# Kernel tuning notes

Hardware: AMD Instinct MI355X
Metric: run time of the kernel (lower is better)

## Reference

```python
import jax, jax.numpy as jnp
import numpy as np

H = 12          # attention heads
NUM_LAYERS = 2  # encoder depth
SCALE = 0.02    # weight init scale


def _ln(x, g, b):
    m = jnp.mean(x, axis=-1, keepdims=True)
    v = jnp.mean((x - m) ** 2, axis=-1, keepdims=True)
    return (x - m) * jax.lax.rsqrt(v + 1e-5) * g + b


def _split_heads(t):
    b, n, d = t.shape
    return t.reshape(b, n, H, d // H).transpose(0, 2, 1, 3)  # (b, h, n, dh)


def _block(p, x, h):
    """Encoder1DBlock: pre-LN elu-linear attention + MLP; returns (x_out, new_hidden)."""
    (lnig, lnib, lnhg, lnhb, lnog, lnob,
     Wqkv, bqkv, Wqkvh, bqkvh, Wout, bout, W1, b1, W2, b2) = p
    xn = _ln(x, lnig, lnib)
    hn = _ln(h, lnhg, lnhb)
    qkv = xn @ Wqkv + bqkv + hn @ Wqkvh + bqkvh            # (b, n, 3d)
    q, k, v = jnp.split(qkv, 3, axis=-1)
    q = jax.nn.elu(_split_heads(q)) + 1.0
    k = jax.nn.elu(_split_heads(k)) + 1.0
    v = _split_heads(v)
    # linear attention: (q k^T) v == q (k^T v); skip the n x n matrix
    kv = jnp.einsum('bhjd,bhje->bhde', k, v)
    o = jnp.einsum('bhid,bhde->bhie', q, kv)
    o = o.transpose(0, 2, 1, 3).reshape(x.shape)
    attn = o @ Wout + bout                                  # to_out
    x2 = attn + x
    y = jax.nn.gelu(_ln(x2, lnog, lnob) @ W1 + b1, approximate=False) @ W2 + b2
    return x2 + y, attn + h


def _encoder(x, hidden, spatial_pos, temporal_pos, params):
    # pos[b,t,j,d] = temporal[b,t,d] * spatial[b,j,d]  (the n=1 einsum in the source)
    pos = temporal_pos[:, :, None, :] * spatial_pos[:, None, :, :]  # (b, L, n, d)
    for idx in range(NUM_LAYERS):
        x = x + pos
        x_t = jnp.moveaxis(x, 1, 0)          # (L, b, n, d)
        # forward direction: hidden gets pos_embedding[:, idx] (layer index, as in source)
        pf = tuple(p[0, idx] for p in params)
        pos_f = pos[:, idx]
        def step_f(h, xt, pf=pf, pos_f=pos_f):
            y, h2 = _block(pf, xt, h + pos_f)
            return h2, y
        _, yf = jax.lax.scan(step_f, hidden, x_t)
        # backward direction: hidden gets the time-indexed pos of the current frame
        pb = tuple(p[1, idx] for p in params)
        pos_t = jnp.moveaxis(pos, 1, 0)
        def step_b(h, inp, pb=pb):
            xt, pt = inp
            y, h2 = _block(pb, xt, h + pt)
            return h2, y
        _, yb = jax.lax.scan(step_b, hidden, (x_t[::-1], pos_t[::-1]))
        x = jnp.moveaxis(yf + yb[::-1], 0, 1)
    return x


def setup_inputs() -> dict:
    key = jax.random.key(0)
    B, L, N, D, M = 2, 12, 1024, 768, 3072
    ks = jax.random.split(key, 16)
    P = (2, NUM_LAYERS)  # (direction, layer)
    w = lambda k, shape: jax.random.normal(k, shape, jnp.float32) * SCALE
    inp = {
        'x': jax.random.normal(ks[0], (B, L, N, D), jnp.float32),
        'hidden': jax.random.normal(ks[1], (B, N, D), jnp.float32),
        'spatial_pos': jax.random.normal(ks[2], (B, N, D), jnp.float32) * 0.02,
        'temporal_pos': jax.random.normal(ks[3], (B, L, D), jnp.float32),
        'lni_g': jnp.ones(P + (D,)), 'lni_b': jnp.zeros(P + (D,)),
        'lnh_g': jnp.ones(P + (D,)), 'lnh_b': jnp.zeros(P + (D,)),
        'lno_g': jnp.ones(P + (D,)), 'lno_b': jnp.zeros(P + (D,)),
        'Wqkv': w(ks[4], P + (D, 3 * D)), 'bqkv': jnp.zeros(P + (3 * D,)),
        'Wqkvh': w(ks[5], P + (D, 3 * D)), 'bqkvh': jnp.zeros(P + (3 * D,)),
        'Wout': w(ks[6], P + (D, D)), 'bout': jnp.zeros(P + (D,)),
        'W1': w(ks[7], P + (D, M)), 'b1': jnp.zeros(P + (M,)),
        'W2': w(ks[8], P + (M, D)), 'b2': jnp.zeros(P + (D,)),
    }
    return inp


def reference(x, hidden, spatial_pos, temporal_pos,
              lni_g, lni_b, lnh_g, lnh_b, lno_g, lno_b,
              Wqkv, bqkv, Wqkvh, bqkvh, Wout, bout, W1, b1, W2, b2):
    params = (lni_g, lni_b, lnh_g, lnh_b, lno_g, lno_b,
              Wqkv, bqkv, Wqkvh, bqkvh, Wout, bout, W1, b1, W2, b2)
    return _encoder(x, hidden, spatial_pos, temporal_pos, params)
```

## Files before the change

kernel.cpp:

```cpp
#include <hip/hip_runtime.h>

#define DEV __device__ __forceinline__
typedef unsigned short u16;
typedef __attribute__((ext_vector_type(8))) __bf16 bf16x8;
typedef __attribute__((ext_vector_type(4))) float f32x4;

constexpr int Ln = 12, Nn = 1024, Dn = 768;

DEV float bf2f(u16 u) { unsigned x = ((unsigned)u) << 16; return __builtin_bit_cast(float, x); }
DEV u16 f2bf(float f) {
    unsigned x = __builtin_bit_cast(unsigned, f);
    x = (x + 0x7fffu + ((x >> 16) & 1u)) >> 16;
    return (u16)x;
}

DEV void gll16(const u16* g, u16* l) {
    __builtin_amdgcn_global_load_lds((const __attribute__((address_space(1))) unsigned*)g,
                                     (__attribute__((address_space(3))) unsigned*)l, 16, 0, 0);
}

DEV float block_sum(float v, float* sred) {
#pragma unroll
    for (int o = 32; o > 0; o >>= 1) v += __shfl_down(v, o, 64);
    int wid = threadIdx.x >> 6, lane = threadIdx.x & 63;
    if (lane == 0) sred[wid] = v;
    __syncthreads();
    v = sred[0] + sred[1] + sred[2] + sred[3];
    __syncthreads();
    return v;
}

__global__ void __launch_bounds__(256) ln1_kernel(
    const float* __restrict__ xf, const u16* __restrict__ xb, float* __restrict__ hbuf,
    const float* __restrict__ temporal, const float* __restrict__ spatial,
    const float* __restrict__ lig, const float* __restrict__ lib,
    const float* __restrict__ lhg, const float* __restrict__ lhb,
    u16* __restrict__ acat, int l, int tF, int tB)
{
    __shared__ float sred[4];
    int r = blockIdx.x, tid = threadIdx.x;
    int dir = r >> 11, b = (r >> 10) & 1, n = r & 1023;
    int t = dir ? tB : tF;
    int tp = dir ? tB : l;
    int so = (dir * 2 + l) * Dn;
    size_t xoff = ((size_t)(b * Ln + t) * Nn + n) * Dn;
    float* hrow = hbuf + (size_t)r * Dn;
    const float* trt = temporal + (size_t)(b * Ln + t) * Dn;
    const float* trh = temporal + (size_t)(b * Ln + tp) * Dn;
    const float* srow = spatial + (size_t)(b * Nn + n) * Dn;
    u16* arow = acat + (size_t)r * (2 * Dn);

    float xv[3], hv[3], sx = 0.f, sh = 0.f;
#pragma unroll
    for (int i = 0; i < 3; i++) {
        int c = tid + i * 256;
        float sp = srow[c];
        float xr = xf ? xf[xoff + c] : bf2f(xb[xoff + c]);
        xv[i] = xr + trt[c] * sp;
        hv[i] = hrow[c] + trh[c] * sp;
        hrow[c] = hv[i];
        sx += xv[i]; sh += hv[i];
    }
    float mx = block_sum(sx, sred) * (1.f / 768.f);
    float mh = block_sum(sh, sred) * (1.f / 768.f);
    float vx = 0.f, vh = 0.f;
#pragma unroll
    for (int i = 0; i < 3; i++) {
        float d = xv[i] - mx; vx += d * d;
        d = hv[i] - mh; vh += d * d;
    }
    vx = block_sum(vx, sred) * (1.f / 768.f);
    vh = block_sum(vh, sred) * (1.f / 768.f);
    float rx = rsqrtf(vx + 1e-5f), rh = rsqrtf(vh + 1e-5f);
#pragma unroll
    for (int i = 0; i < 3; i++) {
        int c = tid + i * 256;
        arow[c]      = f2bf((xv[i] - mx) * rx * lig[so + c] + lib[so + c]);
        arow[Dn + c] = f2bf((hv[i] - mh) * rh * lhg[so + c] + lhb[so + c]);
    }
}

__global__ void __launch_bounds__(256) ln2_kernel(
    const float* __restrict__ x2, const float* __restrict__ g, const float* __restrict__ bb,
    u16* __restrict__ out, int l)
{
    __shared__ float sred[4];
    int r = blockIdx.x, tid = threadIdx.x;
    int dir = r >> 11;
    int so = (dir * 2 + l) * Dn;
    const float* row = x2 + (size_t)r * Dn;
    u16* orow = out + (size_t)r * Dn;
    float v[3], s = 0.f;
#pragma unroll
    for (int i = 0; i < 3; i++) { int c = tid + i * 256; v[i] = row[c]; s += v[i]; }
    float m = block_sum(s, sred) * (1.f / 768.f);
    float va = 0.f;
#pragma unroll
    for (int i = 0; i < 3; i++) { float d = v[i] - m; va += d * d; }
    va = block_sum(va, sred) * (1.f / 768.f);
    float rs = rsqrtf(va + 1e-5f);
#pragma unroll
    for (int i = 0; i < 3; i++) {
        int c = tid + i * 256;
        orow[c] = f2bf((v[i] - m) * rs * g[so + c] + bb[so + c]);
    }
}

struct GArgs {
    const u16* A; int lda;
    const u16* BT; long long bstride; int ldb; int K;
    const float* Wf; const float* Wf2; long long wstride; int ksplit;
    const float* bias1; int b1s;
    const float* bias2; int b2s;
    u16* obf;
    const float* xf; const u16* xb;
    u16* yb; float* yf; int store_flag;
    const float* temp; const float* spat;
    float* x2; float* hbuf;
    int tF, tB;
};

template <int MT, int NT, int MODE, bool CACHED>
__global__ void __launch_bounds__(256) gemm_kernel(GArgs ga)
{
    __shared__ __align__(16) u16 As[MT * 32];
    __shared__ __align__(16) u16 Bs[NT * 32];
    constexpr int FM = MT / 32, FN = NT / 32;
    int tid = threadIdx.x;
    const u16 *A, *Bc = nullptr;
    const float *W1_ = nullptr, *W2_ = nullptr;
    int lda, ldb, K, rowbase, colbase, dir = 0;
    if constexpr (MODE == 1) {
        int combo = blockIdx.y, g4 = combo / 12, h = combo - g4 * 12;
        rowbase = g4 * 1024 + blockIdx.x * MT; colbase = h * 64;
        A = ga.A + (size_t)rowbase * 2304 + h * 64; lda = 2304;
        Bc = ga.BT + (size_t)combo * 4096; ldb = 64; K = 64;
    } else {
        dir = blockIdx.z;
        rowbase = dir * 2048 + blockIdx.x * MT; colbase = blockIdx.y * NT;
        A = ga.A + (size_t)rowbase * ga.lda; lda = ga.lda;
        ldb = ga.ldb; K = ga.K;
        if constexpr (CACHED) {
            Bc = ga.BT + (size_t)dir * ga.bstride + (size_t)colbase * ldb;
        } else {
            W1_ = ga.Wf + (size_t)dir * ga.wstride + colbase;
            if (ga.Wf2) W2_ = ga.Wf2 + (size_t)dir * ga.wstride + colbase;
        }
    }
    int wid = tid >> 6, lane = tid & 63;
    int wm = wid >> 1, wn = wid & 1, lrow = lane & 15, kq = lane >> 4;
    f32x4 acc[FM][FN];
#pragma unroll
    for (int i = 0; i < FM; i++)
#pragma unroll
        for (int j = 0; j < FN; j++) acc[i][j] = f32x4{0.f, 0.f, 0.f, 0.f};

    for (int k0 = 0; k0 < K; k0 += 32) {
#pragma unroll
        for (int p = 0; p < (MT * 64) / 4096; p++) {
            int idx = p * 256 + tid, row = idx >> 2, ch = idx & 3;
            gll16(A + (size_t)row * lda + k0 + ch * 8, As + idx * 8);
        }
        if constexpr (CACHED || MODE == 1) {
#pragma unroll
            for (int p = 0; p < (NT * 64) / 4096; p++) {
                int idx = p * 256 + tid, row = idx >> 2, ch = idx & 3;
                gll16(Bc + (size_t)row * ldb + k0 + ch * 8, Bs + idx * 8);
            }
        } else {
            const float* Wk = (W2_ && k0 >= ga.ksplit) ? W2_ + (size_t)(k0 - ga.ksplit) * ldb
                                                       : W1_ + (size_t)k0 * ldb;
#pragma unroll
            for (int p = 0; p < NT / 32; p++) {
                int u = p * 256 + tid;
                int k = u >> 5, nb = u & 31;
                float4 w = *(const float4*)(Wk + (size_t)k * ldb + nb * 4);
                Bs[(nb * 4 + 0) * 32 + k] = f2bf(w.x);
                Bs[(nb * 4 + 1) * 32 + k] = f2bf(w.y);
                Bs[(nb * 4 + 2) * 32 + k] = f2bf(w.z);
                Bs[(nb * 4 + 3) * 32 + k] = f2bf(w.w);
            }
        }
        __syncthreads();
        bf16x8 av[FM], bv[FN];
#pragma unroll
        for (int i = 0; i < FM; i++)
            av[i] = *(const bf16x8*)(As + (wm * (MT / 2) + i * 16 + lrow) * 32 + kq * 8);
#pragma unroll
        for (int j = 0; j < FN; j++)
            bv[j] = *(const bf16x8*)(Bs + (wn * (NT / 2) + j * 16 + lrow) * 32 + kq * 8);
#pragma unroll
        for (int i = 0; i < FM; i++)
#pragma unroll
            for (int j = 0; j < FN; j++)
                acc[i][j] = __builtin_amdgcn_mfma_f32_16x16x32_bf16(av[i], bv[j], acc[i][j], 0, 0, 0);
        __syncthreads();
    }

    const float* b1 = ga.bias1 ? ga.bias1 + (size_t)dir * ga.b1s : nullptr;
    const float* b2 = ga.bias2 ? ga.bias2 + (size_t)dir * ga.b2s : nullptr;
#pragma unroll
    for (int fm = 0; fm < FM; fm++) {
#pragma unroll
        for (int fn = 0; fn < FN; fn++) {
#pragma unroll
            for (int r2 = 0; r2 < 4; r2++) {
                int row = rowbase + wm * (MT / 2) + fm * 16 + kq * 4 + r2;
                int col = colbase + wn * (NT / 2) + fn * 16 + lrow;
                float v = acc[fm][fn][r2];
                if constexpr (MODE == 0) {
                    v += b1[col] + b2[col];
                    if (col < 1536) v = v > 0.f ? v + 1.f : __expf(v);
                    ga.obf[(size_t)row * 2304 + col] = f2bf(v);
                } else if constexpr (MODE == 1) {
                    ga.obf[(size_t)row * 768 + col] = f2bf(v);
                } else if constexpr (MODE == 2) {
                    v += b1[col];
                    int b = (row >> 10) & 1, n = row & 1023;
                    int t = (row >> 11) ? ga.tB : ga.tF;
                    float pos = ga.temp[(size_t)(b * Ln + t) * Dn + col] *
                                ga.spat[(size_t)(b * Nn + n) * Dn + col];
                    size_t xi = ((size_t)(b * Ln + t) * Nn + n) * Dn + col;
                    float xv = (ga.xf ? ga.xf[xi] : bf2f(ga.xb[xi])) + pos;
                    ga.x2[(size_t)row * Dn + col] = v + xv;
                    ga.hbuf[(size_t)row * Dn + col] += v;
                } else if constexpr (MODE == 3) {
                    v += b1[col];
                    v = 0.5f * v * (1.f + erff(v * 0.7071067811865475f));
                    ga.obf[(size_t)row * 3072 + col] = f2bf(v);
                } else {
                    v += b1[col] + ga.x2[(size_t)row * Dn + col];
                    int b = (row >> 10) & 1, n = row & 1023;
                    int t = (row >> 11) ? ga.tB : ga.tF;
                    size_t oi = ((size_t)(b * Ln + t) * Nn + n) * Dn + col;
                    if (ga.yf) {
                        if (ga.store_flag) ga.yf[oi] = v;
                        else ga.yf[oi] += v;
                    } else {
                        if (ga.store_flag) ga.yb[oi] = f2bf(v);
                        else ga.yb[oi] = f2bf(v + bf2f(ga.yb[oi]));
                    }
                }
            }
        }
    }
}

__global__ void __launch_bounds__(256) kv_partial_kernel(const u16* __restrict__ qkv,
                                                         float* __restrict__ part)
{
    int combo = blockIdx.x, js = blockIdx.y;
    int g4 = combo / 12, h = combo - g4 * 12;
    int d0 = (threadIdx.x & 15) * 4, e0 = (threadIdx.x >> 4) * 4;
    const u16* base = qkv + ((size_t)g4 * 1024 + js * 128) * 2304 + 768 + h * 64;
    float acc[4][4] = {};
#pragma unroll 4
    for (int j = 0; j < 128; j++) {
        const u16* kp = base + (size_t)j * 2304 + d0;
        const u16* vp = base + (size_t)j * 2304 + 768 + e0;
        ushort4 kk = *(const ushort4*)kp;
        ushort4 vv = *(const ushort4*)vp;
        float kd[4] = {bf2f(kk.x), bf2f(kk.y), bf2f(kk.z), bf2f(kk.w)};
        float ve[4] = {bf2f(vv.x), bf2f(vv.y), bf2f(vv.z), bf2f(vv.w)};
#pragma unroll
        for (int di = 0; di < 4; di++)
#pragma unroll
            for (int ei = 0; ei < 4; ei++) acc[di][ei] += kd[di] * ve[ei];
    }
    float* pp = part + ((size_t)js * 48 + combo) * 4096;
#pragma unroll
    for (int di = 0; di < 4; di++)
#pragma unroll
        for (int ei = 0; ei < 4; ei++)
            pp[(e0 + ei) * 64 + (d0 + di)] = acc[di][ei];
}

__global__ void __launch_bounds__(256) kv_reduce_kernel(const float* __restrict__ part,
                                                        u16* __restrict__ kvT)
{
    int combo = blockIdx.x;
    for (int idx = threadIdx.x; idx < 4096; idx += 256) {
        float s = 0.f;
#pragma unroll
        for (int js = 0; js < 8; js++) s += part[((size_t)js * 48 + combo) * 4096 + idx];
        kvT[(size_t)combo * 4096 + idx] = f2bf(s);
    }
}

__global__ void transpose_kernel(const float* __restrict__ src, u16* __restrict__ dst,
                                 int K, int N, int ldd, int dcol)
{
    __shared__ float tile[32][33];
    int n0 = blockIdx.x * 32, k0 = blockIdx.y * 32;
    int tx = threadIdx.x, ty = threadIdx.y;
#pragma unroll
    for (int i = 0; i < 4; i++) {
        int k = k0 + ty + i * 8;
        tile[ty + i * 8][tx] = src[(size_t)k * N + n0 + tx];
    }
    __syncthreads();
#pragma unroll
    for (int i = 0; i < 4; i++) {
        int n = n0 + ty + i * 8;
        dst[(size_t)n * ldd + dcol + k0 + tx] = f2bf(tile[tx][ty + i * 8]);
    }
}

__global__ void __launch_bounds__(256) init_h_kernel(const float* __restrict__ hidden,
                                                     float* __restrict__ hbuf)
{
    unsigned i = blockIdx.x * 256u + threadIdx.x;
    unsigned d = i % 768u;
    unsigned r = i / 768u;
    unsigned b = (r >> 10) & 1u, n = r & 1023u;
    hbuf[i] = hidden[((size_t)b * 1024 + n) * 768 + d];
}

extern "C" void kernel_launch(void* const* d_in, const int* in_sizes, int n_in,
                              void* d_out, int out_size, void* d_ws, size_t ws_size,
                              hipStream_t stream)
{
    (void)in_sizes; (void)n_in; (void)out_size;
    const float* xin    = (const float*)d_in[0];
    const float* hidden = (const float*)d_in[1];
    const float* spat   = (const float*)d_in[2];
    const float* temp   = (const float*)d_in[3];
    const float* lig    = (const float*)d_in[4];
    const float* lib_   = (const float*)d_in[5];
    const float* lhg    = (const float*)d_in[6];
    const float* lhb    = (const float*)d_in[7];
    const float* log_   = (const float*)d_in[8];
    const float* lob    = (const float*)d_in[9];
    const float* Wqkv   = (const float*)d_in[10];
    const float* bqkv   = (const float*)d_in[11];
    const float* Wqkvh  = (const float*)d_in[12];
    const float* bqkvh  = (const float*)d_in[13];
    const float* Wout   = (const float*)d_in[14];
    const float* bout   = (const float*)d_in[15];
    const float* W1     = (const float*)d_in[16];
    const float* b1     = (const float*)d_in[17];
    const float* W2     = (const float*)d_in[18];
    const float* b2     = (const float*)d_in[19];

    char* w = (char*)d_ws;
    float* hbuf  = (float*)(w + 0);
    float* x2    = (float*)(w + 12582912);
    u16*   xC    = (u16*)(w + 25165824);
    u16*   kvT   = (u16*)(w + 62914560);
    u16*   regA  = (u16*)(w + 63307776);
    u16*   regB  = (u16*)(w + 75890688);
    u16*   qkvTc = (u16*)(w + 101056512);
    u16*   woutTc= (u16*)(w + 115212288);
    u16*   w1Tc  = (u16*)(w + 117571584);
    u16*   w2Tc  = (u16*)(w + 127008768);
    const bool cached = ws_size >= 136445952ull;

    u16*   acat  = regA;
    float* kvp   = (float*)regA;
    u16*   obf   = regA;
    u16*   ln2b  = regA + 3145728;
    u16*   qkvb  = regB;
    u16*   mlp1b = regB;

    dim3 tb(32, 8);
    for (int l = 0; l < 2; l++) {
        if (cached) {
            for (int dir = 0; dir < 2; dir++) {
                int s4 = dir * 2 + l;
                transpose_kernel<<<dim3(72, 24), tb, 0, stream>>>(
                    Wqkv + (size_t)s4 * 768 * 2304, qkvTc + (size_t)dir * 2304 * 1536, 768, 2304, 1536, 0);
                transpose_kernel<<<dim3(72, 24), tb, 0, stream>>>(
                    Wqkvh + (size_t)s4 * 768 * 2304, qkvTc + (size_t)dir * 2304 * 1536, 768, 2304, 1536, 768);
                transpose_kernel<<<dim3(24, 24), tb, 0, stream>>>(
                    Wout + (size_t)s4 * 768 * 768, woutTc + (size_t)dir * 768 * 768, 768, 768, 768, 0);
                transpose_kernel<<<dim3(96, 24), tb, 0, stream>>>(
                    W1 + (size_t)s4 * 768 * 3072, w1Tc + (size_t)dir * 3072 * 768, 768, 3072, 768, 0);
                transpose_kernel<<<dim3(24, 96), tb, 0, stream>>>(
                    W2 + (size_t)s4 * 3072 * 768, w2Tc + (size_t)dir * 768 * 3072, 3072, 768, 3072, 0);
            }
        }
        init_h_kernel<<<12288, 256, 0, stream>>>(hidden, hbuf);
        const float* xsf = l ? nullptr : xin;
        const u16*   xsb = l ? xC : nullptr;
        float* yf = l ? (float*)d_out : nullptr;
        u16*   yb = l ? nullptr : xC;
        for (int s = 0; s < 12; s++) {
            int tF = s, tB = 11 - s;
            ln1_kernel<<<4096, 256, 0, stream>>>(xsf, xsb, hbuf, temp, spat, lig, lib_, lhg, lhb,
                                                 acat, l, tF, tB);
            {
                GArgs g{};
                g.A = acat; g.lda = 1536; g.K = 1536;
                g.bias1 = bqkv + (size_t)l * 2304; g.b1s = 2 * 2304;
                g.bias2 = bqkvh + (size_t)l * 2304; g.b2s = 2 * 2304;
                g.obf = qkvb;
                if (cached) {
                    g.BT = qkvTc; g.bstride = 2304ll * 1536; g.ldb = 1536;
                    gemm_kernel<128, 128, 0, true><<<dim3(16, 18, 2), 256, 0, stream>>>(g);
                } else {
                    g.Wf = Wqkv + (size_t)l * 768 * 2304;
                    g.Wf2 = Wqkvh + (size_t)l * 768 * 2304;
                    g.wstride = 2ll * 768 * 2304; g.ksplit = 768; g.ldb = 2304;
                    gemm_kernel<128, 128, 0, false><<<dim3(16, 18, 2), 256, 0, stream>>>(g);
                }
            }
            kv_partial_kernel<<<dim3(48, 8), 256, 0, stream>>>(qkvb, kvp);
            kv_reduce_kernel<<<48, 256, 0, stream>>>(kvp, kvT);
            {
                GArgs g{};
                g.A = qkvb; g.BT = kvT; g.obf = obf;
                gemm_kernel<128, 64, 1, true><<<dim3(8, 48, 1), 256, 0, stream>>>(g);
            }
            {
                GArgs g{};
                g.A = obf; g.lda = 768; g.K = 768;
                g.bias1 = bout + (size_t)l * 768; g.b1s = 2 * 768;
                g.xf = xsf; g.xb = xsb; g.temp = temp; g.spat = spat; g.x2 = x2; g.hbuf = hbuf;
                g.tF = tF; g.tB = tB;
                if (cached) {
                    g.BT = woutTc; g.bstride = 768ll * 768; g.ldb = 768;
                    gemm_kernel<128, 128, 2, true><<<dim3(16, 6, 2), 256, 0, stream>>>(g);
                } else {
                    g.Wf = Wout + (size_t)l * 768 * 768; g.wstride = 2ll * 768 * 768;
                    g.ldb = 768; g.ksplit = g.K;
                    gemm_kernel<128, 128, 2, false><<<dim3(16, 6, 2), 256, 0, stream>>>(g);
                }
            }
            ln2_kernel<<<4096, 256, 0, stream>>>(x2, log_, lob, ln2b, l);
            {
                GArgs g{};
                g.A = ln2b; g.lda = 768; g.K = 768;
                g.bias1 = b1 + (size_t)l * 3072; g.b1s = 2 * 3072;
                g.obf = mlp1b;
                if (cached) {
                    g.BT = w1Tc; g.bstride = 3072ll * 768; g.ldb = 768;
                    gemm_kernel<128, 128, 3, true><<<dim3(16, 24, 2), 256, 0, stream>>>(g);
                } else {
                    g.Wf = W1 + (size_t)l * 768 * 3072; g.wstride = 2ll * 768 * 3072;
                    g.ldb = 3072; g.ksplit = g.K;
                    gemm_kernel<128, 128, 3, false><<<dim3(16, 24, 2), 256, 0, stream>>>(g);
                }
            }
            {
                GArgs g{};
                g.A = mlp1b; g.lda = 3072; g.K = 3072;
                g.bias1 = b2 + (size_t)l * 768; g.b1s = 2 * 768;
                g.x2 = x2; g.yf = yf; g.yb = yb; g.store_flag = (s <= 5) ? 1 : 0;
                g.tF = tF; g.tB = tB;
                if (cached) {
                    g.BT = w2Tc; g.bstride = 768ll * 3072; g.ldb = 3072;
                    gemm_kernel<128, 128, 4, true><<<dim3(16, 6, 2), 256, 0, stream>>>(g);
                } else {
                    g.Wf = W2 + (size_t)l * 3072 * 768; g.wstride = 2ll * 3072 * 768;
                    g.ldb = 768; g.ksplit = g.K;
                    gemm_kernel<128, 128, 4, false><<<dim3(16, 6, 2), 256, 0, stream>>>(g);
                }
            }
        }
    }
}
```

Before: 6.983 ms.

## Double-buffer LDS tiles in cached GEMM path to overlap loads with MFMA

For GEMM variants whose B operand is already bf16 (cached weights or the per-head kv mode), the kernel now keeps two LDS buffers. It issues direct global-to-LDS loads for the next K-step before computing on the current one, and uses an explicit vmcnt wait plus barriers. This is meant to hide global memory latency behind the MFMA work. The cost is twice the LDS footprint for those variants, which may lower occupancy. The uncached fp32-weight path stays single-buffered.

```diff
diff --git a/kernel.cpp b/kernel.cpp
--- a/kernel.cpp
+++ b/kernel.cpp
@@ -123,9 +123,11 @@
 template <int MT, int NT, int MODE, bool CACHED>
 __global__ void __launch_bounds__(256) gemm_kernel(GArgs ga)
 {
-    __shared__ __align__(16) u16 As[MT * 32];
-    __shared__ __align__(16) u16 Bs[NT * 32];
     constexpr int FM = MT / 32, FN = NT / 32;
+    constexpr bool DB = (CACHED || MODE == 1);
+    constexpr int NBUF = DB ? 2 : 1;
+    __shared__ __align__(16) u16 As[NBUF][MT * 32];
+    __shared__ __align__(16) u16 Bs[NBUF][NT * 32];
     int tid = threadIdx.x;
     const u16 *A, *Bc = nullptr;
     const float *W1_ = nullptr, *W2_ = nullptr;
@@ -155,46 +157,85 @@
 #pragma unroll
         for (int j = 0; j < FN; j++) acc[i][j] = f32x4{0.f, 0.f, 0.f, 0.f};
 
-    for (int k0 = 0; k0 < K; k0 += 32) {
-#pragma unroll
-        for (int p = 0; p < (MT * 64) / 4096; p++) {
-            int idx = p * 256 + tid, row = idx >> 2, ch = idx & 3;
-            gll16(A + (size_t)row * lda + k0 + ch * 8, As + idx * 8);
+    if constexpr (DB) {
+        constexpr int AL = (MT * 64) / 4096;
+        constexpr int BL = (NT * 64) / 4096;
+        constexpr int LPS = AL + BL;
+        auto stage = [&](int buf, int k0) {
+#pragma unroll
+            for (int p = 0; p < AL; p++) {
+                int idx = p * 256 + tid, row = idx >> 2, ch = idx & 3;
+                gll16(A + (size_t)row * lda + k0 + ch * 8, As[buf] + idx * 8);
+            }
+#pragma unroll
+            for (int p = 0; p < BL; p++) {
+                int idx = p * 256 + tid, row = idx >> 2, ch = idx & 3;
+                gll16(Bc + (size_t)row * ldb + k0 + ch * 8, Bs[buf] + idx * 8);
+            }
+        };
+        stage(0, 0);
+        const int nk = K >> 5;
+        for (int t = 0; t < nk; t++) {
+            int cur = t & 1;
+            if (t + 1 < nk) {
+                stage(cur ^ 1, (t + 1) << 5);
+                asm volatile("s_waitcnt vmcnt(%0)" :: "n"(LPS) : "memory");
+            } else {
+                asm volatile("s_waitcnt vmcnt(0)" ::: "memory");
+            }
+            __builtin_amdgcn_s_barrier();
+            asm volatile("" ::: "memory");
+            bf16x8 av[FM], bv[FN];
+#pragma unroll
+            for (int i = 0; i < FM; i++)
+                av[i] = *(const bf16x8*)(As[cur] + (wm * (MT / 2) + i * 16 + lrow) * 32 + kq * 8);
+#pragma unroll
+            for (int j = 0; j < FN; j++)
+                bv[j] = *(const bf16x8*)(Bs[cur] + (wn * (NT / 2) + j * 16 + lrow) * 32 + kq * 8);
+#pragma unroll
+            for (int i = 0; i < FM; i++)
+#pragma unroll
+                for (int j = 0; j < FN; j++)
+                    acc[i][j] = __builtin_amdgcn_mfma_f32_16x16x32_bf16(av[i], bv[j], acc[i][j], 0, 0, 0);
+            asm volatile("" ::: "memory");
+            __builtin_amdgcn_s_barrier();
         }
-        if constexpr (CACHED || MODE == 1) {
-#pragma unroll
-            for (int p = 0; p < (NT * 64) / 4096; p++) {
+    } else {
+        for (int k0 = 0; k0 < K; k0 += 32) {
+#pragma unroll
+            for (int p = 0; p < (MT * 64) / 4096; p++) {
                 int idx = p * 256 + tid, row = idx >> 2, ch = idx & 3;
-                gll16(Bc + (size_t)row * ldb + k0 + ch * 8, Bs + idx * 8);
-            }
-        } else {
-            const float* Wk = (W2_ && k0 >= ga.ksplit) ? W2_ + (size_t)(k0 - ga.ksplit) * ldb
-                                                       : W1_ + (size_t)k0 * ldb;
-#pragma unroll
-            for (int p = 0; p < NT / 32; p++) {
-                int u = p * 256 + tid;
-                int k = u >> 5, nb = u & 31;
-                float4 w = *(const float4*)(Wk + (size_t)k * ldb + nb * 4);
-                Bs[(nb * 4 + 0) * 32 + k] = f2bf(w.x);
-                Bs[(nb * 4 + 1) * 32 + k] = f2bf(w.y);
-                Bs[(nb * 4 + 2) * 32 + k] = f2bf(w.z);
-                Bs[(nb * 4 + 3) * 32 + k] = f2bf(w.w);
-            }
+                gll16(A + (size_t)row * lda + k0 + ch * 8, As[0] + idx * 8);
+            }
+            {
+                const float* Wk = (W2_ && k0 >= ga.ksplit) ? W2_ + (size_t)(k0 - ga.ksplit) * ldb
+                                                           : W1_ + (size_t)k0 * ldb;
+#pragma unroll
+                for (int p = 0; p < NT / 32; p++) {
+                    int u = p * 256 + tid;
+                    int k = u >> 5, nb = u & 31;
+                    float4 w = *(const float4*)(Wk + (size_t)k * ldb + nb * 4);
+                    Bs[0][(nb * 4 + 0) * 32 + k] = f2bf(w.x);
+                    Bs[0][(nb * 4 + 1) * 32 + k] = f2bf(w.y);
+                    Bs[0][(nb * 4 + 2) * 32 + k] = f2bf(w.z);
+                    Bs[0][(nb * 4 + 3) * 32 + k] = f2bf(w.w);
+                }
+            }
+            __syncthreads();
+            bf16x8 av[FM], bv[FN];
+#pragma unroll
+            for (int i = 0; i < FM; i++)
+                av[i] = *(const bf16x8*)(As[0] + (wm * (MT / 2) + i * 16 + lrow) * 32 + kq * 8);
+#pragma unroll
+            for (int j = 0; j < FN; j++)
+                bv[j] = *(const bf16x8*)(Bs[0] + (wn * (NT / 2) + j * 16 + lrow) * 32 + kq * 8);
+#pragma unroll
+            for (int i = 0; i < FM; i++)
+#pragma unroll
+                for (int j = 0; j < FN; j++)
+                    acc[i][j] = __builtin_amdgcn_mfma_f32_16x16x32_bf16(av[i], bv[j], acc[i][j], 0, 0, 0);
+            __syncthreads();
         }
-        __syncthreads();
-        bf16x8 av[FM], bv[FN];
-#pragma unroll
-        for (int i = 0; i < FM; i++)
-            av[i] = *(const bf16x8*)(As + (wm * (MT / 2) + i * 16 + lrow) * 32 + kq * 8);
-#pragma unroll
-        for (int j = 0; j < FN; j++)
-            bv[j] = *(const bf16x8*)(Bs + (wn * (NT / 2) + j * 16 + lrow) * 32 + kq * 8);
-#pragma unroll
-        for (int i = 0; i < FM; i++)
-#pragma unroll
-            for (int j = 0; j < FN; j++)
-                acc[i][j] = __builtin_amdgcn_mfma_f32_16x16x32_bf16(av[i], bv[j], acc[i][j], 0, 0, 0);
-        __syncthreads();
     }
 
     const float* b1 = ga.bias1 ? ga.bias1 + (size_t)dir * ga.b1s : nullptr;
```

Result: faster. 6.522 ms (-6.6%).
